# Kernel tuning notes

Measured on AMD Instinct MI355X. Metric: run time of the kernel, lower is better.

## Reference

```python
import jax, jax.numpy as jnp
import numpy as np

EXPERT_CAPACITY = 1024  # per-batch per-expert capacity (token_priority <= capacity)


def setup_inputs() -> dict:
    key = jax.random.key(0)
    ks = jax.random.split(key, 5)
    B, S, D, FF, E = 2, 4096, 1024, 4096, 8
    return {
        "hidden_states": jax.random.normal(ks[0], (B, S, D), dtype=jnp.float32),
        "gate_w": jax.random.normal(ks[1], (D, E), dtype=jnp.float32) * (1.0 / np.sqrt(D)),
        "w1": jax.random.normal(ks[2], (E, D, FF), dtype=jnp.float32) * (1.0 / np.sqrt(D)),
        "w2": jax.random.normal(ks[3], (E, FF, D), dtype=jnp.float32) * (1.0 / np.sqrt(FF)),
        "w3": jax.random.normal(ks[4], (E, D, FF), dtype=jnp.float32) * (1.0 / np.sqrt(D)),
    }


def reference(hidden_states, gate_w, w1, w2, w3):
    B, S, D = hidden_states.shape
    E = gate_w.shape[1]
    C = EXPERT_CAPACITY

    # ---- route (jitter_noise = 0) ----
    router_logits = jnp.einsum("bsd,de->bse", hidden_states, gate_w)  # [B,S,E]
    router_probs = jax.nn.softmax(router_logits, axis=-1)
    sel = jnp.argmax(router_probs, axis=-1)  # [B,S] top-1 expert
    onehot = jax.nn.one_hot(sel, E, dtype=jnp.int32)  # [B,S,E]
    priority = jnp.cumsum(onehot, axis=1)  # cumsum over sequence (dim=-2)
    # position of token in its chosen expert's buffer (0-based)
    pos = jnp.take_along_axis(priority, sel[..., None], axis=-1)[..., 0] - 1  # [B,S]
    keep = pos < C  # token_priority <= expert_capacity
    max_prob = jnp.max(router_probs, axis=-1, keepdims=True)  # [B,S,1]

    # ---- dispatch: scatter kept tokens into [B,E,C,D]; dropped tokens have pos>=C -> mode='drop'
    b_idx = jnp.broadcast_to(jnp.arange(B)[:, None], (B, S))
    buf = jnp.zeros((B, E, C, D), dtype=hidden_states.dtype)
    buf = buf.at[b_idx, sel, pos].set(hidden_states, mode="drop")

    # ---- per-expert gated MLP (grouped GEMM): act(x@w1) * (x@w3) @ w2 ----
    g = jax.nn.silu(jnp.einsum("becd,edf->becf", buf, w1))
    u = jnp.einsum("becd,edf->becf", buf, w3)
    expert_out = jnp.einsum("becf,efd->becd", g * u, w2)  # [B,E,C,D]

    # ---- combine: kept tokens get expert output, dropped tokens keep hidden_states ----
    pos_g = jnp.minimum(pos, C - 1)  # safe gather index for dropped tokens
    gathered = expert_out[b_idx, sel, pos_g]  # [B,S,D]
    next_states = jnp.where(keep[..., None], gathered, hidden_states)
    out = max_prob * next_states  # dropout is identity (p=0)
    return out, router_logits
```

## Files before the change

kernel.cpp:

```cpp
#include <hip/hip_runtime.h>
#include <hip/hip_bf16.h>
#include <stdint.h>

#define B_  2
#define S_  4096
#define D_  1024
#define FF_ 4096
#define E_  8
#define C_  1024

typedef unsigned short u16;
typedef unsigned int   u32;
typedef float f32x4  __attribute__((ext_vector_type(4)));
typedef short bf16x8 __attribute__((ext_vector_type(8)));
typedef u16   u16x8  __attribute__((ext_vector_type(8)));

static __device__ __forceinline__ u16 f2bf(float f) {
    union { float f; u32 u; } v; v.f = f;
    u32 u = v.u;
    u32 r = (u + 0x7FFFu + ((u >> 16) & 1u)) >> 16;
    return (u16)r;
}

static __device__ __forceinline__ void gload_lds16(const u16* g, u16* l) {
    __builtin_amdgcn_global_load_lds(
        (const __attribute__((address_space(1))) u32*)g,
        (__attribute__((address_space(3))) u32*)l, 16, 0, 0);
}

#define BAR()    asm volatile("s_barrier" ::: "memory")
#define WAITV(n) asm volatile("s_waitcnt vmcnt(" #n ")" ::: "memory")
#define WAITL0() do { asm volatile("s_waitcnt lgkmcnt(0)" ::: "memory"); \
                      __builtin_amdgcn_sched_barrier(0); } while (0)

__global__ __launch_bounds__(256) void transpose_cvt(const float* __restrict__ src,
                                                     u16* __restrict__ dst, int K, int N) {
    __shared__ u16 t[64 * 64];
    size_t mat = (size_t)blockIdx.z * K * N;
    int n0 = blockIdx.x * 64, k0 = blockIdx.y * 64;
    int l = threadIdx.x & 63, w = threadIdx.x >> 6;
#pragma unroll
    for (int p = 0; p < 2; ++p) {
        int k = p * 32 + w * 8 + ((l >> 4) << 1);
        int n = (l & 15) * 4;
        float4 v0 = *(const float4*)&src[mat + (size_t)(k0 + k) * N + n0 + n];
        float4 v1 = *(const float4*)&src[mat + (size_t)(k0 + k + 1) * N + n0 + n];
        float a0[4] = {v0.x, v0.y, v0.z, v0.w};
        float a1[4] = {v1.x, v1.y, v1.z, v1.w};
#pragma unroll
        for (int j = 0; j < 4; ++j) {
            int nn = n + j;
            u32 pk = (u32)f2bf(a0[j]) | ((u32)f2bf(a1[j]) << 16);
            int slot = (k >> 3) ^ ((nn & 7) ^ ((nn >> 3) & 7));
            *(u32*)((char*)t + nn * 128 + slot * 16 + (k & 7) * 2) = pk;
        }
    }
    __syncthreads();
#pragma unroll
    for (int p = 0; p < 2; ++p) {
        int n = p * 32 + (threadIdx.x >> 3);
        int k8 = threadIdx.x & 7;
        int slot = k8 ^ ((n & 7) ^ ((n >> 3) & 7));
        u16x8 v = *(u16x8*)((char*)t + n * 128 + slot * 16);
        *(u16x8*)&dst[mat + (size_t)(n0 + n) * K + k0 + k8 * 8] = v;
    }
}

__global__ __launch_bounds__(256) void router_kernel(const float* __restrict__ hidden,
                                                     const float* __restrict__ gate_w,
                                                     float* __restrict__ logits_out,
                                                     int* __restrict__ sel,
                                                     float* __restrict__ maxp) {
    __shared__ float gw[D_ * E_];
    for (int i = threadIdx.x; i < D_ * E_ / 4; i += 256)
        ((float4*)gw)[i] = ((const float4*)gate_w)[i];
    __syncthreads();

    int wave = threadIdx.x >> 6, lane = threadIdx.x & 63;
    int tok = blockIdx.x * 4 + wave;
    const float* hrow = hidden + (size_t)tok * D_;

    double acc[8] = {0, 0, 0, 0, 0, 0, 0, 0};
#pragma unroll 4
    for (int i = 0; i < D_ / 64; i++) {
        int d = i * 64 + lane;
        float h = hrow[d];
        const float4* g4 = (const float4*)(gw + d * 8);
        float4 g0 = g4[0], g1 = g4[1];
        acc[0] += (double)h * g0.x; acc[1] += (double)h * g0.y;
        acc[2] += (double)h * g0.z; acc[3] += (double)h * g0.w;
        acc[4] += (double)h * g1.x; acc[5] += (double)h * g1.y;
        acc[6] += (double)h * g1.z; acc[7] += (double)h * g1.w;
    }
#pragma unroll
    for (int off = 32; off > 0; off >>= 1)
#pragma unroll
        for (int e = 0; e < 8; e++)
            acc[e] += __shfl_xor(acc[e], off);

    float l[8];
#pragma unroll
    for (int e = 0; e < 8; e++) l[e] = (float)acc[e];
    if (lane < 8) logits_out[(size_t)tok * 8 + lane] = l[lane];

    int am = 0; float mx = l[0];
#pragma unroll
    for (int e = 1; e < 8; e++) if (l[e] > mx) { mx = l[e]; am = e; }
    float sum = 0.f;
#pragma unroll
    for (int e = 0; e < 8; e++) sum += expf(l[e] - mx);
    if (lane == 0) { sel[tok] = am; maxp[tok] = 1.0f / sum; }
}

__global__ __launch_bounds__(1024) void scan_kernel(const int* __restrict__ sel,
                                                    int* __restrict__ pos,
                                                    int* __restrict__ slot_token,
                                                    int* __restrict__ counts) {
    __shared__ int hist[16][8];
    __shared__ int base[16][8];
    int b = blockIdx.x;
    int tid = threadIdx.x, wv = tid >> 6, l = tid & 63;
    unsigned long long below = (l == 0) ? 0ull : ((~0ull) >> (64 - l));
    const int* sb = sel + b * S_;

    int eloc[4];
    int cnt[8] = {0, 0, 0, 0, 0, 0, 0, 0};
#pragma unroll
    for (int c = 0; c < 4; c++) {
        int s = wv * 256 + c * 64 + l;
        int e = sb[s];
        eloc[c] = e;
#pragma unroll
        for (int ex = 0; ex < 8; ex++)
            cnt[ex] += (int)__popcll(__ballot(e == ex));
    }
    if (l == 0)
#pragma unroll
        for (int ex = 0; ex < 8; ex++) hist[wv][ex] = cnt[ex];
    __syncthreads();
    if (tid < 128) {
        int ex = tid & 7, v = tid >> 3;
        int s = 0;
        for (int w2 = 0; w2 < v; w2++) s += hist[w2][ex];
        base[v][ex] = s;
        if (v == 15) {
            int tot = s + hist[15][ex];
            counts[b * 8 + ex] = tot < C_ ? tot : C_;
        }
    }
    __syncthreads();
    int carry[8];
#pragma unroll
    for (int ex = 0; ex < 8; ex++) carry[ex] = base[wv][ex];
#pragma unroll
    for (int c = 0; c < 4; c++) {
        int s = wv * 256 + c * 64 + l;
        int e = eloc[c];
        int p = 0;
#pragma unroll
        for (int ex = 0; ex < 8; ex++) {
            unsigned long long m = __ballot(e == ex);
            if (e == ex) p = carry[ex] + (int)__popcll(m & below);
            carry[ex] += (int)__popcll(m);
        }
        pos[b * S_ + s] = p;
        if (p < C_) slot_token[(b * E_ + e) * C_ + p] = s;
    }
}

__global__ __launch_bounds__(256) void gather_kernel(const float* __restrict__ hidden,
                                                     const int* __restrict__ slot_token,
                                                     const int* __restrict__ counts,
                                                     u16* __restrict__ xg) {
    int z = blockIdx.x >> 8;
    int r0 = (blockIdx.x & 255) * 4;
    int cnt = counts[z];
    int slot = r0 + (threadIdx.x >> 6);
    if (slot >= cnt) return;
    int l = threadIdx.x & 63;
    int b = z >> 3;
    int tok = slot_token[z * C_ + slot];
    const float4* src = (const float4*)(hidden + (size_t)(b * S_ + tok) * D_) + l * 4;
    u16x8* dst = (u16x8*)(xg + ((size_t)z * C_ + slot) * D_) + l * 2;
#pragma unroll
    for (int h = 0; h < 2; h++) {
        float4 a = src[h * 2], c = src[h * 2 + 1];
        u16x8 o;
        o[0] = f2bf(a.x); o[1] = f2bf(a.y); o[2] = f2bf(a.z); o[3] = f2bf(a.w);
        o[4] = f2bf(c.x); o[5] = f2bf(c.y); o[6] = f2bf(c.z); o[7] = f2bf(c.w);
        dst[h] = o;
    }
}

__global__ __launch_bounds__(512, 2) void gemm1_kernel(const u16* __restrict__ xg,
                                                       const u16* __restrict__ w1t,
                                                       const u16* __restrict__ w3t,
                                                       const int* __restrict__ counts,
                                                       u16* __restrict__ hbuf) {
    extern __shared__ u16 lds[];
    int phys = blockIdx.x + 32 * (blockIdx.y + 4 * blockIdx.z);
    int virt = (phys & 7) * 256 + (phys >> 3);
    int bx = virt & 31, by = (virt >> 5) & 3, bz = virt >> 7;

    int z = bz;
    int cnt = counts[z];
    int c0 = by * 256;
    if (c0 >= cnt) return;
    int n0 = bx * 128;
    int e = z & 7;

    int tid = threadIdx.x, w = tid >> 6, l = tid & 63;
    int wm = w >> 2, wn = w & 3;

    int arow0 = tid >> 2;
    int lk = ((tid & 3) ^ ((tid >> 3) & 3)) * 8;
    const u16* pA0 = xg + ((size_t)z * C_ + c0 + arow0) * D_ + lk;
    const u16* pA1 = pA0 + (size_t)128 * D_;
    const u16* pB1 = w1t + ((size_t)e * FF_ + n0 + arow0) * D_ + lk;
    const u16* pB3 = w3t + ((size_t)e * FF_ + n0 + arow0) * D_ + lk;
    u32 wA0 = (u32)tid * 8, wA1 = (u32)tid * 8 + 4096;
    u32 wB1 = 8192 + (u32)tid * 8, wB3 = 12288 + (u32)tid * 8;

    u32 ck  = (u32)(((l >> 4) ^ ((l >> 1) & 3)) * 8);
    u32 aoff  = (u32)(wm * 128 + (l & 15)) * 32 + ck;
    u32 b1off = 8192  + (u32)(wn * 32 + (l & 15)) * 32 + ck;
    u32 b3off = 12288 + (u32)(wn * 32 + (l & 15)) * 32 + ck;

    auto STAGE_A = [&](int t) {
        u16* Ls = lds + ((t & 3) << 14);
        int ko = t << 5;
        gload_lds16(pA0 + ko, Ls + wA0);
        gload_lds16(pA1 + ko, Ls + wA1);
    };
    auto STAGE_B = [&](int t) {
        u16* Ls = lds + ((t & 3) << 14);
        int ko = t << 5;
        gload_lds16(pB1 + ko, Ls + wB1);
        gload_lds16(pB3 + ko, Ls + wB3);
    };

    f32x4 acc1[8][2] = {};
    f32x4 acc3[8][2] = {};

    constexpr int NK = D_ / 32;
    STAGE_A(0); STAGE_B(0); STAGE_A(1); STAGE_B(1); STAGE_A(2); STAGE_B(2);
    for (int t = 0; t < NK; ++t) {
        if (t + 2 < NK)      { WAITV(8); }
        else if (t + 1 < NK) { WAITV(4); }
        else                 { WAITV(0); }
        BAR();
        const u16* Ls = lds + ((t & 3) << 14);
        bf16x8 af[8], b1f[2], b3f[2];
#pragma unroll
        for (int f = 0; f < 4; f++) af[f] = *(const bf16x8*)(Ls + aoff + f * 512);
#pragma unroll
        for (int n = 0; n < 2; n++) {
            b1f[n] = *(const bf16x8*)(Ls + b1off + n * 512);
            b3f[n] = *(const bf16x8*)(Ls + b3off + n * 512);
        }
        if (t + 3 < NK) STAGE_A(t + 3);
        WAITL0();
        __builtin_amdgcn_s_setprio(1);
#pragma unroll
        for (int f = 0; f < 4; f++)
#pragma unroll
            for (int n = 0; n < 2; n++) {
                acc1[f][n] = __builtin_amdgcn_mfma_f32_16x16x32_bf16(af[f], b1f[n], acc1[f][n], 0, 0, 0);
                acc3[f][n] = __builtin_amdgcn_mfma_f32_16x16x32_bf16(af[f], b3f[n], acc3[f][n], 0, 0, 0);
            }
        __builtin_amdgcn_s_setprio(0);
        BAR();
#pragma unroll
        for (int f = 4; f < 8; f++) af[f] = *(const bf16x8*)(Ls + aoff + f * 512);
        if (t + 3 < NK) STAGE_B(t + 3);
        WAITL0();
        __builtin_amdgcn_s_setprio(1);
#pragma unroll
        for (int f = 4; f < 8; f++)
#pragma unroll
            for (int n = 0; n < 2; n++) {
                acc1[f][n] = __builtin_amdgcn_mfma_f32_16x16x32_bf16(af[f], b1f[n], acc1[f][n], 0, 0, 0);
                acc3[f][n] = __builtin_amdgcn_mfma_f32_16x16x32_bf16(af[f], b3f[n], acc3[f][n], 0, 0, 0);
            }
        __builtin_amdgcn_s_setprio(0);
    }

#pragma unroll
    for (int f = 0; f < 8; f++) {
        int row = wm * 128 + f * 16 + ((l >> 4) << 2);
#pragma unroll
        for (int rr = 0; rr < 4; rr++) {
            int slot = c0 + row + rr;
            if (slot < cnt) {
                size_t base = ((size_t)z * C_ + slot) * FF_ + n0 + wn * 32 + (l & 15);
#pragma unroll
                for (int n = 0; n < 2; n++) {
                    float g = acc1[f][n][rr], uu = acc3[f][n][rr];
                    float h = (g / (1.f + __expf(-g))) * uu;
                    hbuf[base + n * 16] = f2bf(h);
                }
            }
        }
    }
}

__global__ __launch_bounds__(512, 2) void gemm2_kernel(const u16* __restrict__ hbuf,
                                                       const u16* __restrict__ w2t,
                                                       const int* __restrict__ slot_token,
                                                       const int* __restrict__ counts,
                                                       const float* __restrict__ maxp,
                                                       float* __restrict__ out) {
    extern __shared__ u16 lds[];
    int phys = blockIdx.x + 4 * (blockIdx.y + 4 * blockIdx.z);
    int virt = (phys & 7) * 32 + (phys >> 3);
    int bx = virt & 3, by = (virt >> 2) & 3, bz = virt >> 4;

    int z = bz;
    int cnt = counts[z];
    int c0 = by * 256;
    if (c0 >= cnt) return;
    int n0 = bx * 256;
    int b = z >> 3, e = z & 7;

    int tid = threadIdx.x, w = tid >> 6, l = tid & 63;
    int wm = w >> 2, wn = w & 3;

    int arow0 = tid >> 2;
    int lk = ((tid & 3) ^ ((tid >> 3) & 3)) * 8;
    const u16* pA0 = hbuf + ((size_t)z * C_ + c0 + arow0) * FF_ + lk;
    const u16* pA1 = pA0 + (size_t)128 * FF_;
    const u16* pB0 = w2t + ((size_t)e * D_ + n0 + arow0) * FF_ + lk;
    const u16* pB1 = pB0 + (size_t)128 * FF_;
    u32 wsl = (u32)tid * 8;

    u32 ck  = (u32)(((l >> 4) ^ ((l >> 1) & 3)) * 8);
    u32 aoff = (u32)(wm * 128 + (l & 15)) * 32 + ck;
    u32 boff = 8192 + (u32)(wn * 64 + (l & 15)) * 32 + ck;

    auto STAGE_A = [&](int t) {
        u16* Ls = lds + ((t & 3) << 14);
        int ko = t << 5;
        gload_lds16(pA0 + ko, Ls + wsl);
        gload_lds16(pA1 + ko, Ls + 4096 + wsl);
    };
    auto STAGE_B = [&](int t) {
        u16* Ls = lds + ((t & 3) << 14);
        int ko = t << 5;
        gload_lds16(pB0 + ko, Ls + 8192 + wsl);
        gload_lds16(pB1 + ko, Ls + 12288 + wsl);
    };

    f32x4 acc[8][4] = {};

    constexpr int NK = FF_ / 32;
    STAGE_A(0); STAGE_B(0); STAGE_A(1); STAGE_B(1); STAGE_A(2); STAGE_B(2);
    for (int t = 0; t < NK; ++t) {
        if (t + 2 < NK)      { WAITV(8); }
        else if (t + 1 < NK) { WAITV(4); }
        else                 { WAITV(0); }
        BAR();
        const u16* Ls = lds + ((t & 3) << 14);
        bf16x8 af[8], bfv[4];
#pragma unroll
        for (int f = 0; f < 4; f++) af[f] = *(const bf16x8*)(Ls + aoff + f * 512);
#pragma unroll
        for (int n = 0; n < 4; n++) bfv[n] = *(const bf16x8*)(Ls + boff + n * 512);
        if (t + 3 < NK) STAGE_A(t + 3);
        WAITL0();
        __builtin_amdgcn_s_setprio(1);
#pragma unroll
        for (int f = 0; f < 4; f++)
#pragma unroll
            for (int n = 0; n < 4; n++)
                acc[f][n] = __builtin_amdgcn_mfma_f32_16x16x32_bf16(af[f], bfv[n], acc[f][n], 0, 0, 0);
        __builtin_amdgcn_s_setprio(0);
        BAR();
#pragma unroll
        for (int f = 4; f < 8; f++) af[f] = *(const bf16x8*)(Ls + aoff + f * 512);
        if (t + 3 < NK) STAGE_B(t + 3);
        WAITL0();
        __builtin_amdgcn_s_setprio(1);
#pragma unroll
        for (int f = 4; f < 8; f++)
#pragma unroll
            for (int n = 0; n < 4; n++)
                acc[f][n] = __builtin_amdgcn_mfma_f32_16x16x32_bf16(af[f], bfv[n], acc[f][n], 0, 0, 0);
        __builtin_amdgcn_s_setprio(0);
    }

#pragma unroll
    for (int f = 0; f < 8; f++) {
        int row = wm * 128 + f * 16 + ((l >> 4) << 2);
#pragma unroll
        for (int rr = 0; rr < 4; rr++) {
            int slot = c0 + row + rr;
            if (slot < cnt) {
                int s = slot_token[z * C_ + slot];
                float sc = maxp[b * S_ + s];
                float* orow = out + ((size_t)b * S_ + s) * D_ + n0 + wn * 64 + (l & 15);
#pragma unroll
                for (int n = 0; n < 4; n++)
                    orow[n * 16] = sc * acc[f][n][rr];
            }
        }
    }
}

__global__ __launch_bounds__(256) void combine_dropped(const float* __restrict__ hidden,
                                                       const int* __restrict__ pos,
                                                       const float* __restrict__ maxp,
                                                       float* __restrict__ out) {
    int t = blockIdx.x;
    if (pos[t] < C_) return;
    float sc = maxp[t];
    const float* src = hidden + (size_t)t * D_;
    float* dst = out + (size_t)t * D_;
    for (int d = threadIdx.x; d < D_; d += 256) dst[d] = sc * src[d];
}

extern "C" void kernel_launch(void* const* d_in, const int* in_sizes, int n_in,
                              void* d_out, int out_size, void* d_ws, size_t ws_size,
                              hipStream_t stream) {
    const float* hidden = (const float*)d_in[0];
    const float* gate_w = (const float*)d_in[1];
    const float* w1     = (const float*)d_in[2];
    const float* w2     = (const float*)d_in[3];
    const float* w3     = (const float*)d_in[4];

    float* out        = (float*)d_out;
    float* logits_out = out + (size_t)B_ * S_ * D_;

    char* ws = (char*)d_ws;
    u16* xg        = (u16*)ws;            ws += (size_t)B_ * E_ * C_ * D_ * 2;
    u16* w1t       = (u16*)ws;            ws += (size_t)E_ * D_ * FF_ * 2;
    u16* w3t       = (u16*)ws;            ws += (size_t)E_ * D_ * FF_ * 2;
    u16* w2t       = (u16*)ws;            ws += (size_t)E_ * D_ * FF_ * 2;
    u16* hbuf      = (u16*)ws;            ws += (size_t)B_ * E_ * C_ * FF_ * 2;
    int*   sel        = (int*)ws;         ws += (size_t)B_ * S_ * 4;
    int*   pos        = (int*)ws;         ws += (size_t)B_ * S_ * 4;
    float* maxp       = (float*)ws;       ws += (size_t)B_ * S_ * 4;
    int*   slot_token = (int*)ws;         ws += (size_t)B_ * E_ * C_ * 4;
    int*   counts     = (int*)ws;         ws += (size_t)B_ * E_ * 4;

    (void)hipFuncSetAttribute((const void*)gemm1_kernel,
                              hipFuncAttributeMaxDynamicSharedMemorySize, 131072);
    (void)hipFuncSetAttribute((const void*)gemm2_kernel,
                              hipFuncAttributeMaxDynamicSharedMemorySize, 131072);

    router_kernel<<<B_ * S_ / 4, 256, 0, stream>>>(hidden, gate_w, logits_out, sel, maxp);
    scan_kernel<<<B_, 1024, 0, stream>>>(sel, pos, slot_token, counts);
    gather_kernel<<<B_ * E_ * 256, 256, 0, stream>>>(hidden, slot_token, counts, xg);

    transpose_cvt<<<dim3(FF_ / 64, D_ / 64, E_), 256, 0, stream>>>(w1, w1t, D_, FF_);
    transpose_cvt<<<dim3(FF_ / 64, D_ / 64, E_), 256, 0, stream>>>(w3, w3t, D_, FF_);
    transpose_cvt<<<dim3(D_ / 64, FF_ / 64, E_), 256, 0, stream>>>(w2, w2t, FF_, D_);

    gemm1_kernel<<<dim3(32, 4, 16), 512, 131072, stream>>>(xg, w1t, w3t, counts, hbuf);
    gemm2_kernel<<<dim3(4, 4, 16), 512, 131072, stream>>>(hbuf, w2t, slot_token, counts, maxp, out);
    combine_dropped<<<B_ * S_, 256, 0, stream>>>(hidden, pos, maxp, out);
}
```

Before: 478.4 us.

## Retile gemm1 to 128x128 blocks of 4 waves with a triple-buffered pipeline

Reshapes the fused W1/W3 GEMM from 256-row, 8-wave tiles with a 4-stage LDS ring to 128-row, 4-wave tiles. Each wave now covers all 128 rows and 64 interleaved W1/W3 columns, and the kernel uses a 3-stage buffer in 72KB of LDS, one barrier per k-step, and a flattened 1D grid with a new block remap. The goal is to cut per-block overhead and skip more empty capacity tiles, since the finer row granularity tracks per-expert counts more closely. In exchange, B tiles are reloaded more often per output, and each wave holds 32 accumulators, which raises register pressure.

```diff
diff --git a/kernel.cpp b/kernel.cpp
--- a/kernel.cpp
+++ b/kernel.cpp
@@ -192,112 +192,95 @@
     }
 }
 
-__global__ __launch_bounds__(512, 2) void gemm1_kernel(const u16* __restrict__ xg,
+__global__ __launch_bounds__(256, 2) void gemm1_kernel(const u16* __restrict__ xg,
                                                        const u16* __restrict__ w1t,
                                                        const u16* __restrict__ w3t,
                                                        const int* __restrict__ counts,
                                                        u16* __restrict__ hbuf) {
     extern __shared__ u16 lds[];
-    int phys = blockIdx.x + 32 * (blockIdx.y + 4 * blockIdx.z);
-    int virt = (phys & 7) * 256 + (phys >> 3);
-    int bx = virt & 31, by = (virt >> 5) & 3, bz = virt >> 7;
+    int phys = blockIdx.x;
+    int virt = (phys & 7) * 512 + (phys >> 3);
+    int by = virt & 7, bx = (virt >> 3) & 31, bz = virt >> 8;
 
     int z = bz;
     int cnt = counts[z];
-    int c0 = by * 256;
+    int c0 = by * 128;
     if (c0 >= cnt) return;
     int n0 = bx * 128;
     int e = z & 7;
 
-    int tid = threadIdx.x, w = tid >> 6, l = tid & 63;
-    int wm = w >> 2, wn = w & 3;
-
-    int arow0 = tid >> 2;
-    int lk = ((tid & 3) ^ ((tid >> 3) & 3)) * 8;
-    const u16* pA0 = xg + ((size_t)z * C_ + c0 + arow0) * D_ + lk;
-    const u16* pA1 = pA0 + (size_t)128 * D_;
-    const u16* pB1 = w1t + ((size_t)e * FF_ + n0 + arow0) * D_ + lk;
-    const u16* pB3 = w3t + ((size_t)e * FF_ + n0 + arow0) * D_ + lk;
-    u32 wA0 = (u32)tid * 8, wA1 = (u32)tid * 8 + 4096;
-    u32 wB1 = 8192 + (u32)tid * 8, wB3 = 12288 + (u32)tid * 8;
-
-    u32 ck  = (u32)(((l >> 4) ^ ((l >> 1) & 3)) * 8);
-    u32 aoff  = (u32)(wm * 128 + (l & 15)) * 32 + ck;
-    u32 b1off = 8192  + (u32)(wn * 32 + (l & 15)) * 32 + ck;
-    u32 b3off = 12288 + (u32)(wn * 32 + (l & 15)) * 32 + ck;
-
-    auto STAGE_A = [&](int t) {
-        u16* Ls = lds + ((t & 3) << 14);
+    int tid = threadIdx.x, wn = tid >> 6, l = tid & 63;
+
+    const u16* pA[2];
+#pragma unroll
+    for (int i = 0; i < 2; i++) {
+        int q = i * 256 + tid;
+        int r = q >> 2, pc = q & 3;
+        pA[i] = xg + ((size_t)z * C_ + c0 + r) * D_ + (pc ^ ((r >> 1) & 3)) * 8;
+    }
+    const u16* pB[4];
+#pragma unroll
+    for (int i = 0; i < 4; i++) {
+        int q = i * 256 + tid;
+        int R = q >> 2, pc = q & 3;
+        int panel = (R >> 5) & 1;
+        int ffl = ((R >> 6) << 5) + (R & 31);
+        const u16* wmat = panel ? w3t : w1t;
+        pB[i] = wmat + ((size_t)e * FF_ + n0 + ffl) * D_ + (pc ^ ((R >> 1) & 3)) * 8;
+    }
+    u32 dA = (u32)tid * 8;
+    u32 dB = 4096 + (u32)tid * 8;
+
+    u32 ck = (u32)(((l >> 4) ^ ((l >> 1) & 3)) * 8);
+
+    f32x4 acc[8][4] = {};
+
+    auto STAGE = [&](int t) {
+        u16* Ls = lds + (t % 3) * 12288;
         int ko = t << 5;
-        gload_lds16(pA0 + ko, Ls + wA0);
-        gload_lds16(pA1 + ko, Ls + wA1);
+#pragma unroll
+        for (int i = 0; i < 2; i++) gload_lds16(pA[i] + ko, Ls + dA + i * 2048);
+#pragma unroll
+        for (int i = 0; i < 4; i++) gload_lds16(pB[i] + ko, Ls + dB + i * 2048);
     };
-    auto STAGE_B = [&](int t) {
-        u16* Ls = lds + ((t & 3) << 14);
-        int ko = t << 5;
-        gload_lds16(pB1 + ko, Ls + wB1);
-        gload_lds16(pB3 + ko, Ls + wB3);
-    };
-
-    f32x4 acc1[8][2] = {};
-    f32x4 acc3[8][2] = {};
 
     constexpr int NK = D_ / 32;
-    STAGE_A(0); STAGE_B(0); STAGE_A(1); STAGE_B(1); STAGE_A(2); STAGE_B(2);
+    STAGE(0); STAGE(1);
     for (int t = 0; t < NK; ++t) {
-        if (t + 2 < NK)      { WAITV(8); }
-        else if (t + 1 < NK) { WAITV(4); }
-        else                 { WAITV(0); }
+        if (t + 1 < NK) { WAITV(6); } else { WAITV(0); }
         BAR();
-        const u16* Ls = lds + ((t & 3) << 14);
-        bf16x8 af[8], b1f[2], b3f[2];
-#pragma unroll
-        for (int f = 0; f < 4; f++) af[f] = *(const bf16x8*)(Ls + aoff + f * 512);
-#pragma unroll
-        for (int n = 0; n < 2; n++) {
-            b1f[n] = *(const bf16x8*)(Ls + b1off + n * 512);
-            b3f[n] = *(const bf16x8*)(Ls + b3off + n * 512);
-        }
-        if (t + 3 < NK) STAGE_A(t + 3);
+        const u16* Ls = lds + (t % 3) * 12288;
+        bf16x8 af[8], bf[4];
+#pragma unroll
+        for (int f = 0; f < 8; f++)
+            af[f] = *(const bf16x8*)(Ls + (u32)(f * 16 + (l & 15)) * 32 + ck);
+#pragma unroll
+        for (int j = 0; j < 4; j++)
+            bf[j] = *(const bf16x8*)(Ls + 4096 + (u32)(wn * 64 + j * 16 + (l & 15)) * 32 + ck);
+        if (t + 2 < NK) STAGE(t + 2);
         WAITL0();
         __builtin_amdgcn_s_setprio(1);
 #pragma unroll
-        for (int f = 0; f < 4; f++)
-#pragma unroll
-            for (int n = 0; n < 2; n++) {
-                acc1[f][n] = __builtin_amdgcn_mfma_f32_16x16x32_bf16(af[f], b1f[n], acc1[f][n], 0, 0, 0);
-                acc3[f][n] = __builtin_amdgcn_mfma_f32_16x16x32_bf16(af[f], b3f[n], acc3[f][n], 0, 0, 0);
-            }
+        for (int f = 0; f < 8; f++)
+#pragma unroll
+            for (int j = 0; j < 4; j++)
+                acc[f][j] = __builtin_amdgcn_mfma_f32_16x16x32_bf16(af[f], bf[j], acc[f][j], 0, 0, 0);
         __builtin_amdgcn_s_setprio(0);
-        BAR();
-#pragma unroll
-        for (int f = 4; f < 8; f++) af[f] = *(const bf16x8*)(Ls + aoff + f * 512);
-        if (t + 3 < NK) STAGE_B(t + 3);
-        WAITL0();
-        __builtin_amdgcn_s_setprio(1);
-#pragma unroll
-        for (int f = 4; f < 8; f++)
-#pragma unroll
-            for (int n = 0; n < 2; n++) {
-                acc1[f][n] = __builtin_amdgcn_mfma_f32_16x16x32_bf16(af[f], b1f[n], acc1[f][n], 0, 0, 0);
-                acc3[f][n] = __builtin_amdgcn_mfma_f32_16x16x32_bf16(af[f], b3f[n], acc3[f][n], 0, 0, 0);
-            }
-        __builtin_amdgcn_s_setprio(0);
     }
 
 #pragma unroll
     for (int f = 0; f < 8; f++) {
-        int row = wm * 128 + f * 16 + ((l >> 4) << 2);
-#pragma unroll
-        for (int rr = 0; rr < 4; rr++) {
-            int slot = c0 + row + rr;
-            if (slot < cnt) {
-                size_t base = ((size_t)z * C_ + slot) * FF_ + n0 + wn * 32 + (l & 15);
-#pragma unroll
-                for (int n = 0; n < 2; n++) {
-                    float g = acc1[f][n][rr], uu = acc3[f][n][rr];
+        int rb = c0 + f * 16 + ((l >> 4) << 2);
+#pragma unroll
+        for (int j = 0; j < 2; j++) {
+            int ff = n0 + wn * 32 + j * 16 + (l & 15);
+#pragma unroll
+            for (int r = 0; r < 4; r++) {
+                int slot = rb + r;
+                if (slot < cnt) {
+                    float g = acc[f][j][r], uu = acc[f][j + 2][r];
                     float h = (g / (1.f + __expf(-g))) * uu;
-                    hbuf[base + n * 16] = f2bf(h);
+                    hbuf[((size_t)z * C_ + slot) * FF_ + ff] = f2bf(h);
                 }
             }
         }
@@ -443,7 +426,7 @@
     int*   counts     = (int*)ws;         ws += (size_t)B_ * E_ * 4;
 
     (void)hipFuncSetAttribute((const void*)gemm1_kernel,
-                              hipFuncAttributeMaxDynamicSharedMemorySize, 131072);
+                              hipFuncAttributeMaxDynamicSharedMemorySize, 73728);
     (void)hipFuncSetAttribute((const void*)gemm2_kernel,
                               hipFuncAttributeMaxDynamicSharedMemorySize, 131072);
 
@@ -455,7 +438,7 @@
     transpose_cvt<<<dim3(FF_ / 64, D_ / 64, E_), 256, 0, stream>>>(w3, w3t, D_, FF_);
     transpose_cvt<<<dim3(D_ / 64, FF_ / 64, E_), 256, 0, stream>>>(w2, w2t, FF_, D_);
 
-    gemm1_kernel<<<dim3(32, 4, 16), 512, 131072, stream>>>(xg, w1t, w3t, counts, hbuf);
+    gemm1_kernel<<<4096, 256, 73728, stream>>>(xg, w1t, w3t, counts, hbuf);
     gemm2_kernel<<<dim3(4, 4, 16), 512, 131072, stream>>>(hbuf, w2t, slot_token, counts, maxp, out);
     combine_dropped<<<B_ * S_, 256, 0, stream>>>(hidden, pos, maxp, out);
 }
```

Measured after the change: 474.5 us. No clear change (-0.8%).

## Fuse bf16 conversion into router and gather token rows inside gemm1

Applied to the files above, without the earlier changes.

The router kernel now writes a bf16 copy of every hidden row as it reads it, and the separate gather kernel is removed. gemm1 instead looks up slot_token to find its A-operand rows and loads them directly from the bf16 hidden copy. This removes one kernel launch and a second full read of the fp32 hidden states. In exchange, the router's scalar 2-byte stores may be poorly coalesced, and gemm1's A loads become indirect row gathers.

```diff
diff --git a/kernel.cpp b/kernel.cpp
--- a/kernel.cpp
+++ b/kernel.cpp
@@ -70,7 +70,8 @@
                                                      const float* __restrict__ gate_w,
                                                      float* __restrict__ logits_out,
                                                      int* __restrict__ sel,
-                                                     float* __restrict__ maxp) {
+                                                     float* __restrict__ maxp,
+                                                     u16* __restrict__ xbf) {
     __shared__ float gw[D_ * E_];
     for (int i = threadIdx.x; i < D_ * E_ / 4; i += 256)
         ((float4*)gw)[i] = ((const float4*)gate_w)[i];
@@ -79,12 +80,14 @@
     int wave = threadIdx.x >> 6, lane = threadIdx.x & 63;
     int tok = blockIdx.x * 4 + wave;
     const float* hrow = hidden + (size_t)tok * D_;
+    u16* xrow = xbf + (size_t)tok * D_;
 
     double acc[8] = {0, 0, 0, 0, 0, 0, 0, 0};
 #pragma unroll 4
     for (int i = 0; i < D_ / 64; i++) {
         int d = i * 64 + lane;
         float h = hrow[d];
+        xrow[d] = f2bf(h);
         const float4* g4 = (const float4*)(gw + d * 8);
         float4 g0 = g4[0], g1 = g4[1];
         acc[0] += (double)h * g0.x; acc[1] += (double)h * g0.y;
@@ -168,33 +171,10 @@
     }
 }
 
-__global__ __launch_bounds__(256) void gather_kernel(const float* __restrict__ hidden,
-                                                     const int* __restrict__ slot_token,
-                                                     const int* __restrict__ counts,
-                                                     u16* __restrict__ xg) {
-    int z = blockIdx.x >> 8;
-    int r0 = (blockIdx.x & 255) * 4;
-    int cnt = counts[z];
-    int slot = r0 + (threadIdx.x >> 6);
-    if (slot >= cnt) return;
-    int l = threadIdx.x & 63;
-    int b = z >> 3;
-    int tok = slot_token[z * C_ + slot];
-    const float4* src = (const float4*)(hidden + (size_t)(b * S_ + tok) * D_) + l * 4;
-    u16x8* dst = (u16x8*)(xg + ((size_t)z * C_ + slot) * D_) + l * 2;
-#pragma unroll
-    for (int h = 0; h < 2; h++) {
-        float4 a = src[h * 2], c = src[h * 2 + 1];
-        u16x8 o;
-        o[0] = f2bf(a.x); o[1] = f2bf(a.y); o[2] = f2bf(a.z); o[3] = f2bf(a.w);
-        o[4] = f2bf(c.x); o[5] = f2bf(c.y); o[6] = f2bf(c.z); o[7] = f2bf(c.w);
-        dst[h] = o;
-    }
-}
-
-__global__ __launch_bounds__(512, 2) void gemm1_kernel(const u16* __restrict__ xg,
+__global__ __launch_bounds__(512, 2) void gemm1_kernel(const u16* __restrict__ x,
                                                        const u16* __restrict__ w1t,
                                                        const u16* __restrict__ w3t,
+                                                       const int* __restrict__ slot_token,
                                                        const int* __restrict__ counts,
                                                        u16* __restrict__ hbuf) {
     extern __shared__ u16 lds[];
@@ -207,15 +187,18 @@
     int c0 = by * 256;
     if (c0 >= cnt) return;
     int n0 = bx * 128;
-    int e = z & 7;
+    int b = z >> 3, e = z & 7;
 
     int tid = threadIdx.x, w = tid >> 6, l = tid & 63;
     int wm = w >> 2, wn = w & 3;
 
-    int arow0 = tid >> 2;
+    int arow0 = tid >> 2, arow1 = arow0 + 128;
     int lk = ((tid & 3) ^ ((tid >> 3) & 3)) * 8;
-    const u16* pA0 = xg + ((size_t)z * C_ + c0 + arow0) * D_ + lk;
-    const u16* pA1 = pA0 + (size_t)128 * D_;
+    int as0 = c0 + arow0, as1 = c0 + arow1;
+    int tok0 = slot_token[z * C_ + (as0 < cnt ? as0 : 0)];
+    int tok1 = slot_token[z * C_ + (as1 < cnt ? as1 : 0)];
+    const u16* pA0 = x + ((size_t)(b * S_ + tok0)) * D_ + lk;
+    const u16* pA1 = x + ((size_t)(b * S_ + tok1)) * D_ + lk;
     const u16* pB1 = w1t + ((size_t)e * FF_ + n0 + arow0) * D_ + lk;
     const u16* pB3 = w3t + ((size_t)e * FF_ + n0 + arow0) * D_ + lk;
     u32 wA0 = (u32)tid * 8, wA1 = (u32)tid * 8 + 4096;
@@ -431,7 +414,7 @@
     float* logits_out = out + (size_t)B_ * S_ * D_;
 
     char* ws = (char*)d_ws;
-    u16* xg        = (u16*)ws;            ws += (size_t)B_ * E_ * C_ * D_ * 2;
+    u16* hidden_bf = (u16*)ws;            ws += (size_t)B_ * S_ * D_ * 2;
     u16* w1t       = (u16*)ws;            ws += (size_t)E_ * D_ * FF_ * 2;
     u16* w3t       = (u16*)ws;            ws += (size_t)E_ * D_ * FF_ * 2;
     u16* w2t       = (u16*)ws;            ws += (size_t)E_ * D_ * FF_ * 2;
@@ -447,15 +430,14 @@
     (void)hipFuncSetAttribute((const void*)gemm2_kernel,
                               hipFuncAttributeMaxDynamicSharedMemorySize, 131072);
 
-    router_kernel<<<B_ * S_ / 4, 256, 0, stream>>>(hidden, gate_w, logits_out, sel, maxp);
+    router_kernel<<<B_ * S_ / 4, 256, 0, stream>>>(hidden, gate_w, logits_out, sel, maxp, hidden_bf);
     scan_kernel<<<B_, 1024, 0, stream>>>(sel, pos, slot_token, counts);
-    gather_kernel<<<B_ * E_ * 256, 256, 0, stream>>>(hidden, slot_token, counts, xg);
 
     transpose_cvt<<<dim3(FF_ / 64, D_ / 64, E_), 256, 0, stream>>>(w1, w1t, D_, FF_);
     transpose_cvt<<<dim3(FF_ / 64, D_ / 64, E_), 256, 0, stream>>>(w3, w3t, D_, FF_);
     transpose_cvt<<<dim3(D_ / 64, FF_ / 64, E_), 256, 0, stream>>>(w2, w2t, FF_, D_);
 
-    gemm1_kernel<<<dim3(32, 4, 16), 512, 131072, stream>>>(xg, w1t, w3t, counts, hbuf);
+    gemm1_kernel<<<dim3(32, 4, 16), 512, 131072, stream>>>(hidden_bf, w1t, w3t, slot_token, counts, hbuf);
     gemm2_kernel<<<dim3(4, 4, 16), 512, 131072, stream>>>(hbuf, w2t, slot_token, counts, maxp, out);
     combine_dropped<<<B_ * S_, 256, 0, stream>>>(hidden, pos, maxp, out);
 }
```

Measured after the change: 468.3 us. 1.02x faster.
